# Kernel tuning notes

Measured on AMD Instinct MI355X. Metric: run time of the kernel, lower is better.

The kernel has to match this reference:

```python
import jax, jax.numpy as jnp
import numpy as np

EPS = 1e-5  # PyTorch BatchNorm2d default eps


def _batchnorm(x, gamma, beta):
    # training-mode BN over (N, T, V) per channel; x: [N, C, T, V]
    mean = jnp.mean(x, axis=(0, 2, 3), keepdims=True)
    var = jnp.var(x, axis=(0, 2, 3), keepdims=True)
    inv = jax.lax.rsqrt(var + EPS)
    return (x - mean) * inv * gamma[None, :, None, None] + beta[None, :, None, None]


def setup_inputs() -> dict:
    key = jax.random.key(0)
    ks = jax.random.split(key, 8)
    N, Cin, Cout, T, V, S = 64, 64, 128, 300, 25, 3
    x = jax.random.normal(ks[0], (N, Cin, T, V), dtype=jnp.float32)
    A = jax.random.uniform(ks[1], (S, V, V), dtype=jnp.float32)
    # per-subset 1x1 conv weights/biases (kaiming-ish scale)
    W = jax.random.normal(ks[2], (S, Cout, Cin), dtype=jnp.float32) / np.sqrt(Cin)
    b = jax.random.normal(ks[3], (S, Cout), dtype=jnp.float32) * 0.01
    alpha = jnp.zeros((1,), dtype=jnp.float32)
    bn_gamma = jnp.ones((Cout,), dtype=jnp.float32)
    bn_beta = jnp.zeros((Cout,), dtype=jnp.float32)
    # residual down path (in_channels != out_channels): conv1x1 + BN
    down_W = jax.random.normal(ks[4], (Cout, Cin), dtype=jnp.float32) / np.sqrt(Cin)
    down_b = jax.random.normal(ks[5], (Cout,), dtype=jnp.float32) * 0.01
    down_gamma = jnp.ones((Cout,), dtype=jnp.float32)
    down_beta = jnp.zeros((Cout,), dtype=jnp.float32)
    return {
        "x": x, "A": A, "W": W, "b": b, "alpha": alpha,
        "bn_gamma": bn_gamma, "bn_beta": bn_beta,
        "down_W": down_W, "down_b": down_b,
        "down_gamma": down_gamma, "down_beta": down_beta,
    }


def reference(x, A, W, b, alpha, bn_gamma, bn_beta, down_W, down_b, down_gamma, down_beta):
    V = x.shape[-1]
    eye = jnp.eye(V, dtype=x.dtype)
    A_adj = A + alpha[0] * eye[None]  # [S, V, V]
    # sum_s conv1x1_s( x @ A_s ): fuse adjacency matmul, 1x1 conv, subset sum
    y_agg = jnp.einsum('nctv,svw,soc->notw', x, A_adj, W)
    y_agg = y_agg + jnp.sum(b, axis=0)[None, :, None, None]
    y = _batchnorm(y_agg, bn_gamma, bn_beta)
    # residual down: 1x1 conv + BN (in_channels != out_channels)
    res = jnp.einsum('nctv,oc->notv', x, down_W) + down_b[None, :, None, None]
    res = _batchnorm(res, down_gamma, down_beta)
    return jax.nn.relu(y + res)
```

## Files before the change

### kernel.cpp

```cpp
#include <hip/hip_runtime.h>
#include <hip/hip_bf16.h>

#define N_   64
#define CIN  64
#define COUT 128
#define T_   300
#define V_   25
#define S_   3
#define NTV  (N_ * T_ * V_)

#define TS     10
#define NTB    (T_ / TS)
#define NBLK   (N_ * NTB)
#define RED_ROWS   64
#define RED_BLOCKS (NBLK / RED_ROWS)

#define WS_P    0
#define WS_P2   (WS_P + NBLK * 512)
#define WS_COEF (WS_P2 + RED_BLOCKS * 512)
#define WS_WF   (WS_COEF + 512)
#define WS_WSF  (WS_WF + 16384)
#define WS_AF   (WS_WSF + 16384)

typedef __attribute__((ext_vector_type(8))) short short8;
typedef __attribute__((ext_vector_type(4))) float f32x4;

#define LDS_BARRIER() asm volatile("s_waitcnt lgkmcnt(0)\n\ts_barrier" ::: "memory")

__device__ __forceinline__ unsigned short bfbits(float f) {
    union { __hip_bfloat16 h; unsigned short u; } cv;
    cv.h = __float2bfloat16(f);
    return cv.u;
}
__device__ __forceinline__ unsigned int pack2(float lo, float hi) {
    return (unsigned int)bfbits(lo) | ((unsigned int)bfbits(hi) << 16);
}

__device__ __forceinline__ int zoff(int nl, int k) {
    int slot = (k >> 3) ^ (nl & 31);
    return nl * 512 + slot * 16 + (k & 7) * 2;
}

__global__ __launch_bounds__(256) void k_prep(const float* __restrict__ W,
                                              const float* __restrict__ dW,
                                              const float* __restrict__ A,
                                              const float* __restrict__ alpha,
                                              unsigned short* __restrict__ Wf,
                                              unsigned short* __restrict__ Af) {
    int i = blockIdx.x * 256 + threadIdx.x;
    {
        int j = i & 7, lane = (i >> 3) & 63, ks = (i >> 9) & 7;
        int of = (i >> 12) & 1, oh = i >> 13;
        int o = oh * 32 + of * 16 + (lane & 15);
        int k = ks * 32 + (lane >> 4) * 8 + j;
        float wv = (k < 192) ? W[(k >> 6) * (COUT * CIN) + o * CIN + (k & 63)]
                             : dW[o * CIN + (k - 192)];
        Wf[i] = bfbits(wv);
    }
    if (i < 4096) {
        int j = i & 7, lane = (i >> 3) & 63, wf = (i >> 9) & 1, s = i >> 10;
        int v = (lane >> 4) * 8 + j, w = wf * 16 + (lane & 15);
        float av;
        if (s < 3)
            av = (v < V_ && w < V_)
                   ? A[(s * V_ + v) * V_ + w] + ((v == w) ? alpha[0] : 0.f)
                   : 0.f;
        else
            av = (v == w && v < V_) ? 1.f : 0.f;
        Af[i] = bfbits(av);
    }
}

__global__ __launch_bounds__(256) void k_prep2(const float* __restrict__ W,
                                               const float* __restrict__ dW,
                                               const float* __restrict__ coef,
                                               unsigned short* __restrict__ Wsf) {
    int i = blockIdx.x * 256 + threadIdx.x;
    int j = i & 7, lane = (i >> 3) & 63, ks = (i >> 9) & 7;
    int of = (i >> 12) & 1, oh = i >> 13;
    int o = oh * 32 + of * 16 + (lane & 15);
    int k = ks * 32 + (lane >> 4) * 8 + j;
    float wv = (k < 192) ? W[(k >> 6) * (COUT * CIN) + o * CIN + (k & 63)]
                         : dW[o * CIN + (k - 192)];
    float sc = (k < 192) ? coef[o] : coef[COUT + o];
    Wsf[i] = bfbits(wv * sc);
}

struct XRaw { f32x4 a0, a1; float s; };

__device__ __forceinline__ XRaw load_raw(const float* __restrict__ base, int lq) {
    XRaw r;
    if (lq < 3) {
        r.a0 = *(const f32x4*)(base + lq * 8);
        r.a1 = *(const f32x4*)(base + lq * 8 + 4);
        r.s = 0.f;
    } else {
        r.s = base[24];
        r.a0 = (f32x4){0.f, 0.f, 0.f, 0.f};
        r.a1 = (f32x4){0.f, 0.f, 0.f, 0.f};
    }
    return r;
}

__device__ __forceinline__ short8 cvt_xfr(const XRaw& x, int lq) {
    short8 r;
    if (lq < 3) {
#pragma unroll
        for (int j = 0; j < 4; ++j) {
            r[j]     = (short)bfbits(x.a0[j]);
            r[4 + j] = (short)bfbits(x.a1[j]);
        }
    } else {
        r[0] = (short)bfbits(x.s);
#pragma unroll
        for (int j = 1; j < 8; ++j) r[j] = 0;
    }
    return r;
}

__device__ __forceinline__ void stage(char* zb, const unsigned short* Alds,
                                      short8 xfr, int oh, int lq, int lr, int lane) {
    const f32x4 zero = {0.f, 0.f, 0.f, 0.f};
#pragma unroll
    for (int s = 0; s < 4; ++s)
#pragma unroll
        for (int wf = 0; wf < 2; ++wf) {
            short8 af = *(const short8*)(Alds + ((s * 2 + wf) * 64 + lane) * 8);
            f32x4 d = __builtin_amdgcn_mfma_f32_16x16x32_bf16(xfr, af, zero, 0, 0, 0);
            unsigned long long pk = (unsigned long long)pack2(d[0], d[1])
                                  | ((unsigned long long)pack2(d[2], d[3]) << 32);
            int row = wf * 16 + lr;
            int k = s * 64 + oh * 16 + lq * 4;
            *(unsigned long long*)(zb + zoff(row, k)) = pk;
        }
}

template<bool STATS>
__global__ __launch_bounds__(256, 3) void k_gemm(
    const float* __restrict__ x, const unsigned short* __restrict__ Wf,
    const unsigned short* __restrict__ Af, const float* __restrict__ coef,
    float* __restrict__ P, float* __restrict__ out)
{
    __shared__ __align__(16) unsigned short Zt[2][32 * 256];
    __shared__ __align__(16) unsigned short Alds[8 * 64 * 8];

    const int tid = threadIdx.x;
    const int oh = tid >> 6, lane = tid & 63;
    const int lq = lane >> 4, lr = lane & 15;

    const int bid = blockIdx.x;
    const int n = bid / NTB, tb = bid % NTB;
    const int t0 = tb * TS;

    for (int i = tid; i < 512; i += 256)
        *(short8*)(Alds + i * 8) = *(const short8*)(Af + i * 8);

    short8 wfr[2][8];
#pragma unroll
    for (int of = 0; of < 2; ++of)
#pragma unroll
        for (int ks = 0; ks < 8; ++ks)
            wfr[of][ks] = *(const short8*)(Wf + (((oh * 2 + of) * 8 + ks) * 64 + lane) * 8);

    float c0v[2] = {0.f, 0.f};
    if (!STATS) {
        c0v[0] = coef[2 * COUT + oh * 32 + lr];
        c0v[1] = coef[2 * COUT + oh * 32 + 16 + lr];
    }

    float sy[2] = {0.f, 0.f}, sy2[2] = {0.f, 0.f};
    float sr[2] = {0.f, 0.f}, sr2[2] = {0.f, 0.f};

    const int c = oh * 16 + lr;
    const float* xrow = x + ((size_t)(n * CIN + c) * T_) * V_;

    LDS_BARRIER();

    {
        XRaw r0 = load_raw(xrow + (size_t)t0 * V_, lq);
        stage((char*)Zt[0], Alds, cvt_xfr(r0, lq), oh, lq, lr, lane);
    }
    XRaw slotA = load_raw(xrow + (size_t)(t0 + 1) * V_, lq);

    const f32x4 zero = {0.f, 0.f, 0.f, 0.f};

    for (int tt = 0; tt < TS; ++tt) {
        const int t = t0 + tt;
        char* zb = (char*)Zt[tt & 1];
        LDS_BARRIER();

        XRaw slotB;
        if (tt + 2 < TS) slotB = load_raw(xrow + (size_t)(t + 2) * V_, lq);
        else { slotB.a0 = zero; slotB.a1 = zero; slotB.s = 0.f; }

        if (tt + 1 < TS)
            stage((char*)Zt[(tt + 1) & 1], Alds, cvt_xfr(slotA, lq), oh, lq, lr, lane);

        f32x4 acc[2][2], accr[2][2];
#pragma unroll
        for (int ks = 0; ks < 8; ++ks) {
            short8 za[2];
            za[0] = *(const short8*)(zb + zoff(lr, ks * 32 + lq * 8));
            za[1] = *(const short8*)(zb + zoff(16 + lr, ks * 32 + lq * 8));
            if constexpr (STATS) {
                if (ks < 6) {
#pragma unroll
                    for (int mf = 0; mf < 2; ++mf)
#pragma unroll
                        for (int of = 0; of < 2; ++of)
                            acc[mf][of] = __builtin_amdgcn_mfma_f32_16x16x32_bf16(
                                za[mf], wfr[of][ks], ks == 0 ? zero : acc[mf][of], 0, 0, 0);
                } else {
#pragma unroll
                    for (int mf = 0; mf < 2; ++mf)
#pragma unroll
                        for (int of = 0; of < 2; ++of)
                            accr[mf][of] = __builtin_amdgcn_mfma_f32_16x16x32_bf16(
                                za[mf], wfr[of][ks], ks == 6 ? zero : accr[mf][of], 0, 0, 0);
                }
            } else {
#pragma unroll
                for (int mf = 0; mf < 2; ++mf)
#pragma unroll
                    for (int of = 0; of < 2; ++of)
                        acc[mf][of] = __builtin_amdgcn_mfma_f32_16x16x32_bf16(
                            za[mf], wfr[of][ks], ks == 0 ? zero : acc[mf][of], 0, 0, 0);
            }
        }

        if constexpr (STATS) {
#pragma unroll
            for (int of = 0; of < 2; ++of)
#pragma unroll
                for (int mf = 0; mf < 2; ++mf)
#pragma unroll
                    for (int r = 0; r < 4; ++r) {
                        float yv = acc[mf][of][r];
                        sy[of] += yv; sy2[of] = fmaf(yv, yv, sy2[of]);
                        float rv = accr[mf][of][r];
                        sr[of] += rv; sr2[of] = fmaf(rv, rv, sr2[of]);
                    }
        } else {
#pragma unroll
            for (int of = 0; of < 2; ++of) {
                int o = oh * 32 + of * 16 + lr;
                float* rowp = out + ((size_t)(n * COUT + o) * T_ + t) * V_;
                f32x4 v0;
#pragma unroll
                for (int r = 0; r < 4; ++r) v0[r] = fmaxf(acc[0][of][r] + c0v[of], 0.f);
                *(f32x4*)(rowp + lq * 4) = v0;
                if (lq < 2) {
                    f32x4 v1;
#pragma unroll
                    for (int r = 0; r < 4; ++r) v1[r] = fmaxf(acc[1][of][r] + c0v[of], 0.f);
                    *(f32x4*)(rowp + 16 + lq * 4) = v1;
                } else if (lq == 2) {
                    rowp[24] = fmaxf(acc[1][of][0] + c0v[of], 0.f);
                }
            }
        }

        slotA.a0 = slotB.a0; slotA.a1 = slotB.a1; slotA.s = slotB.s;
    }

    if constexpr (STATS) {
#pragma unroll
        for (int of = 0; of < 2; ++of) {
            sy[of]  += __shfl_xor(sy[of], 16);  sy[of]  += __shfl_xor(sy[of], 32);
            sy2[of] += __shfl_xor(sy2[of], 16); sy2[of] += __shfl_xor(sy2[of], 32);
            sr[of]  += __shfl_xor(sr[of], 16);  sr[of]  += __shfl_xor(sr[of], 32);
            sr2[of] += __shfl_xor(sr2[of], 16); sr2[of] += __shfl_xor(sr2[of], 32);
        }
        if (lq == 0) {
            float* p = P + (size_t)bid * 512;
#pragma unroll
            for (int of = 0; of < 2; ++of) {
                int o = oh * 32 + of * 16 + lr;
                p[o] = sy[of]; p[128 + o] = sy2[of];
                p[256 + o] = sr[of]; p[384 + o] = sr2[of];
            }
        }
    }
}

__global__ __launch_bounds__(256) void k_red(const float* __restrict__ P,
                                             float* __restrict__ P2) {
    const int tid = threadIdx.x;
    float a0 = 0.f, a1 = 0.f;
    const int row0 = blockIdx.x * RED_ROWS;
    for (int r = 0; r < RED_ROWS; ++r) {
        const float* p = P + (size_t)(row0 + r) * 512;
        a0 += p[tid];
        a1 += p[256 + tid];
    }
    P2[blockIdx.x * 512 + tid] = a0;
    P2[blockIdx.x * 512 + 256 + tid] = a1;
}

__global__ __launch_bounds__(128) void k_coef(
    const float* __restrict__ P2, const float* __restrict__ gamma,
    const float* __restrict__ beta, const float* __restrict__ dgamma,
    const float* __restrict__ dbeta, const float* __restrict__ b,
    const float* __restrict__ db, float* __restrict__ coef) {
    const int o = threadIdx.x;
    float sy = 0.f, sy2 = 0.f, sr = 0.f, sr2 = 0.f;
    for (int r2 = 0; r2 < RED_BLOCKS; ++r2) {
        const float* p = P2 + r2 * 512;
        sy += p[o]; sy2 += p[128 + o]; sr += p[256 + o]; sr2 += p[384 + o];
    }
    const float bsum = b[o] + b[COUT + o] + b[2 * COUT + o];
    const float dbo = db[o];
    float syb  = sy + (float)NTV * bsum;
    float sy2b = sy2 + 2.f * bsum * sy + (float)NTV * bsum * bsum;
    float srb  = sr + (float)NTV * dbo;
    float sr2b = sr2 + 2.f * dbo * sr + (float)NTV * dbo * dbo;
    const float invn = 1.f / (float)NTV;
    float my = syb * invn, mr = srb * invn;
    float vy = fmaf(-my, my, sy2b * invn);
    float vr = fmaf(-mr, mr, sr2b * invn);
    float ay = rsqrtf(vy + 1e-5f) * gamma[o];
    float ar = rsqrtf(vr + 1e-5f) * dgamma[o];
    float c0 = beta[o] - my * ay + dbeta[o] - mr * ar + ay * bsum + ar * dbo;
    coef[o] = ay; coef[COUT + o] = ar; coef[2 * COUT + o] = c0;
}

extern "C" void kernel_launch(void* const* d_in, const int* in_sizes, int n_in,
                              void* d_out, int out_size, void* d_ws, size_t ws_size,
                              hipStream_t stream) {
    const float* x      = (const float*)d_in[0];
    const float* A      = (const float*)d_in[1];
    const float* W      = (const float*)d_in[2];
    const float* b      = (const float*)d_in[3];
    const float* alpha  = (const float*)d_in[4];
    const float* gamma  = (const float*)d_in[5];
    const float* beta   = (const float*)d_in[6];
    const float* dW     = (const float*)d_in[7];
    const float* db     = (const float*)d_in[8];
    const float* dgamma = (const float*)d_in[9];
    const float* dbeta  = (const float*)d_in[10];

    float* ws   = (float*)d_ws;
    float* P    = ws + WS_P;
    float* P2   = ws + WS_P2;
    float* coef = ws + WS_COEF;
    unsigned short* Wf  = (unsigned short*)(ws + WS_WF);
    unsigned short* Wsf = (unsigned short*)(ws + WS_WSF);
    unsigned short* Af  = (unsigned short*)(ws + WS_AF);
    float* out  = (float*)d_out;

    k_prep<<<128, 256, 0, stream>>>(W, dW, A, alpha, Wf, Af);
    k_gemm<true><<<NBLK, 256, 0, stream>>>(x, Wf, Af, nullptr, P, nullptr);
    k_red<<<RED_BLOCKS, 256, 0, stream>>>(P, P2);
    k_coef<<<1, 128, 0, stream>>>(P2, gamma, beta, dgamma, dbeta, b, db, coef);
    k_prep2<<<128, 256, 0, stream>>>(W, dW, coef, Wsf);
    k_gemm<false><<<NBLK, 256, 0, stream>>>(x, Wsf, Af, coef, nullptr, out);
}
```

Before: 224.8 us.

## Split GEMM block work across 8 waves with one output fragment per wave

```diff
diff --git a/kernel.cpp b/kernel.cpp
--- a/kernel.cpp
+++ b/kernel.cpp
@@ -50,8 +50,8 @@
     int i = blockIdx.x * 256 + threadIdx.x;
     {
         int j = i & 7, lane = (i >> 3) & 63, ks = (i >> 9) & 7;
-        int of = (i >> 12) & 1, oh = i >> 13;
-        int o = oh * 32 + of * 16 + (lane & 15);
+        int oh2 = i >> 12;
+        int o = oh2 * 16 + (lane & 15);
         int k = ks * 32 + (lane >> 4) * 8 + j;
         float wv = (k < 192) ? W[(k >> 6) * (COUT * CIN) + o * CIN + (k & 63)]
                              : dW[o * CIN + (k - 192)];
@@ -77,8 +77,8 @@
                                                unsigned short* __restrict__ Wsf) {
     int i = blockIdx.x * 256 + threadIdx.x;
     int j = i & 7, lane = (i >> 3) & 63, ks = (i >> 9) & 7;
-    int of = (i >> 12) & 1, oh = i >> 13;
-    int o = oh * 32 + of * 16 + (lane & 15);
+    int oh2 = i >> 12;
+    int o = oh2 * 16 + (lane & 15);
     int k = ks * 32 + (lane >> 4) * 8 + j;
     float wv = (k < 192) ? W[(k >> 6) * (COUT * CIN) + o * CIN + (k & 63)]
                          : dW[o * CIN + (k - 192)];
@@ -119,10 +119,12 @@
 }
 
 __device__ __forceinline__ void stage(char* zb, const unsigned short* Alds,
-                                      short8 xfr, int oh, int lq, int lr, int lane) {
+                                      short8 xfr, int sp, int cq,
+                                      int lq, int lr, int lane) {
     const f32x4 zero = {0.f, 0.f, 0.f, 0.f};
 #pragma unroll
-    for (int s = 0; s < 4; ++s)
+    for (int i = 0; i < 2; ++i) {
+        const int s = 2 * sp + i;
 #pragma unroll
         for (int wf = 0; wf < 2; ++wf) {
             short8 af = *(const short8*)(Alds + ((s * 2 + wf) * 64 + lane) * 8);
@@ -130,13 +132,14 @@
             unsigned long long pk = (unsigned long long)pack2(d[0], d[1])
                                   | ((unsigned long long)pack2(d[2], d[3]) << 32);
             int row = wf * 16 + lr;
-            int k = s * 64 + oh * 16 + lq * 4;
+            int k = s * 64 + cq * 16 + lq * 4;
             *(unsigned long long*)(zb + zoff(row, k)) = pk;
         }
+    }
 }
 
 template<bool STATS>
-__global__ __launch_bounds__(256, 3) void k_gemm(
+__global__ __launch_bounds__(512, 4) void k_gemm(
     const float* __restrict__ x, const unsigned short* __restrict__ Wf,
     const unsigned short* __restrict__ Af, const float* __restrict__ coef,
     float* __restrict__ P, float* __restrict__ out)
@@ -145,40 +148,37 @@
     __shared__ __align__(16) unsigned short Alds[8 * 64 * 8];
 
     const int tid = threadIdx.x;
-    const int oh = tid >> 6, lane = tid & 63;
+    const int wid = tid >> 6, lane = tid & 63;
     const int lq = lane >> 4, lr = lane & 15;
+    const int oh2 = wid;
+    const int cq = wid & 3;
+    const int sp = wid >> 2;
 
     const int bid = blockIdx.x;
     const int n = bid / NTB, tb = bid % NTB;
     const int t0 = tb * TS;
 
-    for (int i = tid; i < 512; i += 256)
-        *(short8*)(Alds + i * 8) = *(const short8*)(Af + i * 8);
-
-    short8 wfr[2][8];
-#pragma unroll
-    for (int of = 0; of < 2; ++of)
-#pragma unroll
-        for (int ks = 0; ks < 8; ++ks)
-            wfr[of][ks] = *(const short8*)(Wf + (((oh * 2 + of) * 8 + ks) * 64 + lane) * 8);
-
-    float c0v[2] = {0.f, 0.f};
-    if (!STATS) {
-        c0v[0] = coef[2 * COUT + oh * 32 + lr];
-        c0v[1] = coef[2 * COUT + oh * 32 + 16 + lr];
-    }
-
-    float sy[2] = {0.f, 0.f}, sy2[2] = {0.f, 0.f};
-    float sr[2] = {0.f, 0.f}, sr2[2] = {0.f, 0.f};
-
-    const int c = oh * 16 + lr;
+    if (tid < 512)
+        *(short8*)(Alds + tid * 8) = *(const short8*)(Af + tid * 8);
+
+    short8 wfr[8];
+#pragma unroll
+    for (int ks = 0; ks < 8; ++ks)
+        wfr[ks] = *(const short8*)(Wf + (((oh2 * 8 + ks) * 64 + lane)) * 8);
+
+    float c0v = 0.f;
+    if (!STATS) c0v = coef[2 * COUT + oh2 * 16 + lr];
+
+    float sy = 0.f, sy2 = 0.f, sr = 0.f, sr2 = 0.f;
+
+    const int c = cq * 16 + lr;
     const float* xrow = x + ((size_t)(n * CIN + c) * T_) * V_;
 
     LDS_BARRIER();
 
     {
         XRaw r0 = load_raw(xrow + (size_t)t0 * V_, lq);
-        stage((char*)Zt[0], Alds, cvt_xfr(r0, lq), oh, lq, lr, lane);
+        stage((char*)Zt[0], Alds, cvt_xfr(r0, lq), sp, cq, lq, lr, lane);
     }
     XRaw slotA = load_raw(xrow + (size_t)(t0 + 1) * V_, lq);
 
@@ -194,9 +194,9 @@
         else { slotB.a0 = zero; slotB.a1 = zero; slotB.s = 0.f; }
 
         if (tt + 1 < TS)
-            stage((char*)Zt[(tt + 1) & 1], Alds, cvt_xfr(slotA, lq), oh, lq, lr, lane);
-
-        f32x4 acc[2][2], accr[2][2];
+            stage((char*)Zt[(tt + 1) & 1], Alds, cvt_xfr(slotA, lq), sp, cq, lq, lr, lane);
+
+        f32x4 acc[2], accr[2];
 #pragma unroll
         for (int ks = 0; ks < 8; ++ks) {
             short8 za[2];
@@ -206,57 +206,46 @@
                 if (ks < 6) {
 #pragma unroll
                     for (int mf = 0; mf < 2; ++mf)
-#pragma unroll
-                        for (int of = 0; of < 2; ++of)
-                            acc[mf][of] = __builtin_amdgcn_mfma_f32_16x16x32_bf16(
-                                za[mf], wfr[of][ks], ks == 0 ? zero : acc[mf][of], 0, 0, 0);
+                        acc[mf] = __builtin_amdgcn_mfma_f32_16x16x32_bf16(
+                            za[mf], wfr[ks], ks == 0 ? zero : acc[mf], 0, 0, 0);
                 } else {
 #pragma unroll
                     for (int mf = 0; mf < 2; ++mf)
-#pragma unroll
-                        for (int of = 0; of < 2; ++of)
-                            accr[mf][of] = __builtin_amdgcn_mfma_f32_16x16x32_bf16(
-                                za[mf], wfr[of][ks], ks == 6 ? zero : accr[mf][of], 0, 0, 0);
+                        accr[mf] = __builtin_amdgcn_mfma_f32_16x16x32_bf16(
+                            za[mf], wfr[ks], ks == 6 ? zero : accr[mf], 0, 0, 0);
                 }
             } else {
 #pragma unroll
                 for (int mf = 0; mf < 2; ++mf)
-#pragma unroll
-                    for (int of = 0; of < 2; ++of)
-                        acc[mf][of] = __builtin_amdgcn_mfma_f32_16x16x32_bf16(
-                            za[mf], wfr[of][ks], ks == 0 ? zero : acc[mf][of], 0, 0, 0);
+                    acc[mf] = __builtin_amdgcn_mfma_f32_16x16x32_bf16(
+                        za[mf], wfr[ks], ks == 0 ? zero : acc[mf], 0, 0, 0);
             }
         }
 
         if constexpr (STATS) {
 #pragma unroll
-            for (int of = 0; of < 2; ++of)
-#pragma unroll
-                for (int mf = 0; mf < 2; ++mf)
-#pragma unroll
-                    for (int r = 0; r < 4; ++r) {
-                        float yv = acc[mf][of][r];
-                        sy[of] += yv; sy2[of] = fmaf(yv, yv, sy2[of]);
-                        float rv = accr[mf][of][r];
-                        sr[of] += rv; sr2[of] = fmaf(rv, rv, sr2[of]);
-                    }
+            for (int mf = 0; mf < 2; ++mf)
+#pragma unroll
+                for (int r = 0; r < 4; ++r) {
+                    float yv = acc[mf][r];
+                    sy += yv; sy2 = fmaf(yv, yv, sy2);
+                    float rv = accr[mf][r];
+                    sr += rv; sr2 = fmaf(rv, rv, sr2);
+                }
         } else {
-#pragma unroll
-            for (int of = 0; of < 2; ++of) {
-                int o = oh * 32 + of * 16 + lr;
-                float* rowp = out + ((size_t)(n * COUT + o) * T_ + t) * V_;
-                f32x4 v0;
-#pragma unroll
-                for (int r = 0; r < 4; ++r) v0[r] = fmaxf(acc[0][of][r] + c0v[of], 0.f);
-                *(f32x4*)(rowp + lq * 4) = v0;
-                if (lq < 2) {
-                    f32x4 v1;
-#pragma unroll
-                    for (int r = 0; r < 4; ++r) v1[r] = fmaxf(acc[1][of][r] + c0v[of], 0.f);
-                    *(f32x4*)(rowp + 16 + lq * 4) = v1;
-                } else if (lq == 2) {
-                    rowp[24] = fmaxf(acc[1][of][0] + c0v[of], 0.f);
-                }
+            const int o = oh2 * 16 + lr;
+            float* rowp = out + ((size_t)(n * COUT + o) * T_ + t) * V_;
+            f32x4 v0;
+#pragma unroll
+            for (int r = 0; r < 4; ++r) v0[r] = fmaxf(acc[0][r] + c0v, 0.f);
+            *(f32x4*)(rowp + lq * 4) = v0;
+            if (lq < 2) {
+                f32x4 v1;
+#pragma unroll
+                for (int r = 0; r < 4; ++r) v1[r] = fmaxf(acc[1][r] + c0v, 0.f);
+                *(f32x4*)(rowp + 16 + lq * 4) = v1;
+            } else if (lq == 2) {
+                rowp[24] = fmaxf(acc[1][0] + c0v, 0.f);
             }
         }
 
@@ -264,21 +253,15 @@
     }
 
     if constexpr (STATS) {
-#pragma unroll
-        for (int of = 0; of < 2; ++of) {
-            sy[of]  += __shfl_xor(sy[of], 16);  sy[of]  += __shfl_xor(sy[of], 32);
-            sy2[of] += __shfl_xor(sy2[of], 16); sy2[of] += __shfl_xor(sy2[of], 32);
-            sr[of]  += __shfl_xor(sr[of], 16);  sr[of]  += __shfl_xor(sr[of], 32);
-            sr2[of] += __shfl_xor(sr2[of], 16); sr2[of] += __shfl_xor(sr2[of], 32);
-        }
+        sy  += __shfl_xor(sy, 16);  sy  += __shfl_xor(sy, 32);
+        sy2 += __shfl_xor(sy2, 16); sy2 += __shfl_xor(sy2, 32);
+        sr  += __shfl_xor(sr, 16);  sr  += __shfl_xor(sr, 32);
+        sr2 += __shfl_xor(sr2, 16); sr2 += __shfl_xor(sr2, 32);
         if (lq == 0) {
             float* p = P + (size_t)bid * 512;
-#pragma unroll
-            for (int of = 0; of < 2; ++of) {
-                int o = oh * 32 + of * 16 + lr;
-                p[o] = sy[of]; p[128 + o] = sy2[of];
-                p[256 + o] = sr[of]; p[384 + o] = sr2[of];
-            }
+            const int o = oh2 * 16 + lr;
+            p[o] = sy; p[128 + o] = sy2;
+            p[256 + o] = sr; p[384 + o] = sr2;
         }
     }
 }
@@ -349,9 +332,9 @@
     float* out  = (float*)d_out;
 
     k_prep<<<128, 256, 0, stream>>>(W, dW, A, alpha, Wf, Af);
-    k_gemm<true><<<NBLK, 256, 0, stream>>>(x, Wf, Af, nullptr, P, nullptr);
+    k_gemm<true><<<NBLK, 512, 0, stream>>>(x, Wf, Af, nullptr, P, nullptr);
     k_red<<<RED_BLOCKS, 256, 0, stream>>>(P, P2);
     k_coef<<<1, 128, 0, stream>>>(P2, gamma, beta, dgamma, dbeta, b, db, coef);
     k_prep2<<<128, 256, 0, stream>>>(W, dW, coef, Wsf);
-    k_gemm<false><<<NBLK, 256, 0, stream>>>(x, Wsf, Af, coef, nullptr, out);
-}
+    k_gemm<false><<<NBLK, 512, 0, stream>>>(x, Wsf, Af, coef, nullptr, out);
+}
```

New measurement: 224.6 us. No clear change (-0.1%).
